# Performance work log

Hardware: AMD Instinct MI355X
Metric: run time of the kernel (lower is better)

The kernel has to match this reference:

```python
import jax, jax.numpy as jnp
import numpy as np

# model hyperparameters (from init_kwargs)
N_IN = 2048
NN = 512
BATCH = 64
DT, TAU_M, TAU_X = 0.05, 10.0, 2.0
ALPHA = 1.0 - DT / TAU_M   # membrane decay
BETA = 1.0 - DT / TAU_X    # lateral-trace decay
V_TH = 2.0


def _loo_idx(nn):
    # leave-one-out gather indices: idx[j, n] = j if j < n else j + 1
    j = np.arange(nn - 1)[:, None]
    n = np.arange(nn)[None, :]
    return jnp.asarray(j + (j >= n))  # (nn-1, nn) int


def setup_inputs() -> dict:
    key = jax.random.key(0)
    k1, k2, k3, k4 = jax.random.split(key, 4)
    x = jax.random.uniform(k1, (BATCH, N_IN, NN), dtype=jnp.float32)      # per-neuron external input
    v = jax.random.normal(k2, (BATCH, NN), dtype=jnp.float32)             # membrane state
    z = jnp.zeros((BATCH, NN), dtype=jnp.float32)                         # previous spikes
    z_out = jax.random.uniform(k3, (BATCH, NN), dtype=jnp.float32)        # lateral spike trace
    w = jax.random.normal(k4, (N_IN + NN - 1, NN), dtype=jnp.float32) / np.sqrt(N_IN)
    return {"x": x, "v": v, "z": z, "z_out": z_out, "w": w}


def reference(x, v, z, z_out, w):
    # update lateral trace: z_out = beta * z_out + z (z detached in original)
    z_out_new = BETA * z_out + z
    # leave-one-out lateral input: z_loo[b, j, n] = z_out_new[b, j + (j >= n)]
    idx = _loo_idx(NN)
    z_loo = z_out_new[:, idx]  # (B, NN-1, NN)
    # membrane drive: sum_k x_tot[b,k,n] * w[k,n], where x_tot = cat([x, z_loo], dim=1)
    drive = (jnp.einsum('bkn,kn->bn', x, w[:N_IN])
             + jnp.einsum('bjn,jn->bn', z_loo, w[N_IN:]))
    v_new = ALPHA * v + drive - V_TH * z
    # thresholding nonlinearity -> output spikes
    z_new = (v_new - V_TH > 0).astype(v.dtype)
    return v_new, z_new, z_out_new
```

## Files before the change

### kernel.cpp

```cpp
#include <hip/hip_runtime.h>

#define BATCH 64
#define N_IN  2048
#define NN    512
#define G     4
#define ALPHA 0.995f
#define BETA  0.975f
#define V_TH  2.0f

__global__ __launch_bounds__(1024, 8)
void k1_stream(const float* __restrict__ x, const float* __restrict__ w,
               const float* __restrict__ z, const float* __restrict__ z_out,
               float4* __restrict__ ws)
{
    __shared__ __align__(16) float4 red[G][8][128];
    const int kr  = blockIdx.x;
    const int b0  = blockIdx.y * G;
    const int tid = threadIdx.x;
    const int c4  = tid & 127;
    const int kl  = tid >> 7;

    const float4* __restrict__ x4 = (const float4*)x;
    const float4* __restrict__ w4 = (const float4*)w;
    const int k0 = kr * 64 + kl;

    size_t xoff[G];
#pragma unroll
    for (int g = 0; g < G; ++g)
        xoff[g] = ((size_t)(b0 + g) * N_IN + k0) * 128 + c4;
    size_t woff = (size_t)k0 * 128 + c4;
    const size_t kstep = 8 * 128;

    float4 acc[G];
#pragma unroll
    for (int g = 0; g < G; ++g) acc[g] = make_float4(0.f, 0.f, 0.f, 0.f);

#pragma unroll 2
    for (int i = 0; i < 8; ++i) {
        float4 xv[G];
#pragma unroll
        for (int g = 0; g < G; ++g) xv[g] = x4[xoff[g]];
        const float4 wv = w4[woff];
#pragma unroll
        for (int g = 0; g < G; ++g) {
            acc[g].x += xv[g].x * wv.x;
            acc[g].y += xv[g].y * wv.y;
            acc[g].z += xv[g].z * wv.z;
            acc[g].w += xv[g].w * wv.w;
        }
#pragma unroll
        for (int g = 0; g < G; ++g) xoff[g] += kstep;
        woff += kstep;
    }

#pragma unroll
    for (int g = 0; g < G; ++g) red[g][kl][c4] = acc[g];
    __syncthreads();

    float4 s = make_float4(0.f, 0.f, 0.f, 0.f);
    if (tid < 512) {
        const int g = tid >> 7, c = tid & 127;
        s = red[g][0][c];
#pragma unroll
        for (int l = 1; l < 8; ++l) {
            const float4 o = red[g][l][c];
            s.x += o.x; s.y += o.y; s.z += o.z; s.w += o.w;
        }
    }
    __syncthreads();

    float* d2l = (float*)red;
    float* zr  = d2l + G * NN;
    const int j0 = kr * 16;

    if (tid < G * 17) {
        const int g = tid / 17, jj = tid % 17;
        const int idx = j0 + jj;
        if (idx < NN)
            zr[g * 17 + jj] = BETA * z_out[(b0 + g) * NN + idx]
                            + z[(b0 + g) * NN + idx];
    }
    __syncthreads();

    {
        const int n  = tid & 511;
        const int gh = tid >> 9;
        float p0 = 0.f, p1 = 0.f;
        const int jend = (j0 + 16 < NN - 1) ? j0 + 16 : NN - 1;
        for (int j = j0; j < jend; ++j) {
            const float wv = w[(size_t)(N_IN + j) * NN + n];
            const int jj = j + (j >= n) - j0;
            p0 += zr[(gh * 2 + 0) * 17 + jj] * wv;
            p1 += zr[(gh * 2 + 1) * 17 + jj] * wv;
        }
        d2l[(gh * 2 + 0) * NN + n] = p0;
        d2l[(gh * 2 + 1) * NN + n] = p1;
    }
    __syncthreads();

    if (tid < 512) {
        const int g = tid >> 7, c = tid & 127;
        s.x += d2l[g * NN + 4 * c + 0];
        s.y += d2l[g * NN + 4 * c + 1];
        s.z += d2l[g * NN + 4 * c + 2];
        s.w += d2l[g * NN + 4 * c + 3];
        ws[((size_t)kr * BATCH + b0 + g) * 128 + c] = s;
    }
}

__global__ __launch_bounds__(128)
void k3_epi(const float* __restrict__ v, const float* __restrict__ z,
            const float* __restrict__ z_out, const float* __restrict__ ws,
            float* __restrict__ out)
{
    const int i = blockIdx.x * 128 + threadIdx.x;
    float d = 0.f;
#pragma unroll
    for (int kr = 0; kr < 32; ++kr)
        d += ws[(size_t)kr * (BATCH * NN) + i];
    const float zz = z[i];
    const float vn = ALPHA * v[i] + d - V_TH * zz;
    out[i]                  = vn;
    out[BATCH * NN + i]     = (vn - V_TH > 0.f) ? 1.f : 0.f;
    out[2 * BATCH * NN + i] = BETA * z_out[i] + zz;
}

__global__ __launch_bounds__(1024, 8)
void k1_fallback(const float* __restrict__ x, const float* __restrict__ w,
                 float4* __restrict__ ws)
{
    const int nc  = blockIdx.x;
    const int b0  = blockIdx.y * G;
    const int kr  = blockIdx.z;
    const int tid = threadIdx.x;
    const int nl  = tid & 15;
    const int kk  = tid >> 4;
    const int wid  = tid >> 6;
    const int lane = tid & 63;

    const float4* __restrict__ x4 = (const float4*)x;
    const float4* __restrict__ w4 = (const float4*)w;
    const int c4    = nc * 16 + nl;
    const int kbase = kr * 512 + kk;

    size_t xoff[G];
#pragma unroll
    for (int g = 0; g < G; ++g)
        xoff[g] = ((size_t)(b0 + g) * N_IN + kbase) * 128 + c4;
    size_t woff = (size_t)kbase * 128 + c4;
    const size_t kstep = (size_t)64 * 128;

    float4 acc[G];
#pragma unroll
    for (int g = 0; g < G; ++g) acc[g] = make_float4(0.f, 0.f, 0.f, 0.f);

#pragma unroll 2
    for (int i = 0; i < 8; ++i) {
        float4 xv[G];
#pragma unroll
        for (int g = 0; g < G; ++g) xv[g] = x4[xoff[g]];
        const float4 wv = w4[woff];
#pragma unroll
        for (int g = 0; g < G; ++g) {
            acc[g].x += xv[g].x * wv.x;
            acc[g].y += xv[g].y * wv.y;
            acc[g].z += xv[g].z * wv.z;
            acc[g].w += xv[g].w * wv.w;
        }
#pragma unroll
        for (int g = 0; g < G; ++g) xoff[g] += kstep;
        woff += kstep;
    }

#pragma unroll
    for (int off = 32; off >= 16; off >>= 1) {
#pragma unroll
        for (int g = 0; g < G; ++g) {
            acc[g].x += __shfl_down(acc[g].x, off);
            acc[g].y += __shfl_down(acc[g].y, off);
            acc[g].z += __shfl_down(acc[g].z, off);
            acc[g].w += __shfl_down(acc[g].w, off);
        }
    }

    __shared__ float4 wpart[16][G][16];
    if (lane < 16) {
#pragma unroll
        for (int g = 0; g < G; ++g) wpart[wid][g][lane] = acc[g];
    }
    __syncthreads();

    if (tid < 64) {
        const int g = tid >> 4, c = tid & 15;
        float4 sf = wpart[0][g][c];
#pragma unroll
        for (int ww = 1; ww < 16; ++ww) {
            const float4 o = wpart[ww][g][c];
            sf.x += o.x; sf.y += o.y; sf.z += o.z; sf.w += o.w;
        }
        ws[((size_t)kr * BATCH + b0 + g) * 128 + nc * 16 + c] = sf;
    }
}

__global__ __launch_bounds__(1024)
void k2_finish(const float* __restrict__ v, const float* __restrict__ z,
               const float* __restrict__ z_out, const float* __restrict__ w,
               const float* __restrict__ ws, float* __restrict__ out)
{
    const int nc  = blockIdx.x;
    const int b   = blockIdx.y;
    const int nb  = nc * 64;
    const int tid = threadIdx.x;

    __shared__ float zlds[NN];
    __shared__ float r2[1024];

    if (tid < NN)
        zlds[tid] = BETA * z_out[b * NN + tid] + z[b * NN + tid];
    __syncthreads();

    const int n_loc = tid & 63;
    const int n     = nb + n_loc;
    const int jg    = tid >> 6;
    float d2 = 0.f;
#pragma unroll 4
    for (int j = jg; j < NN - 1; j += 16)
        d2 += zlds[j + (j >= n)] * w[(size_t)(N_IN + j) * NN + n];
    r2[tid] = d2;
    __syncthreads();

    if (tid < 64) {
        float d1 = 0.f;
#pragma unroll
        for (int kr = 0; kr < 4; ++kr)
            d1 += ws[((size_t)kr * BATCH + b) * NN + n];
        float d2s = 0.f;
#pragma unroll
        for (int g = 0; g < 16; ++g) d2s += r2[g * 64 + n_loc];
        const float vv    = v[b * NN + n];
        const float zz    = z[b * NN + n];
        const float v_new = ALPHA * vv + d1 + d2s - V_TH * zz;
        out[b * NN + n]                  = v_new;
        out[BATCH * NN + b * NN + n]     = (v_new - V_TH > 0.f) ? 1.f : 0.f;
        out[2 * BATCH * NN + b * NN + n] = zlds[n];
    }
}

extern "C" void kernel_launch(void* const* d_in, const int* in_sizes, int n_in,
                              void* d_out, int out_size, void* d_ws, size_t ws_size,
                              hipStream_t stream) {
    (void)in_sizes; (void)n_in; (void)out_size;
    const float* x     = (const float*)d_in[0];
    const float* v     = (const float*)d_in[1];
    const float* z     = (const float*)d_in[2];
    const float* z_out = (const float*)d_in[3];
    const float* w     = (const float*)d_in[4];
    float* out = (float*)d_out;
    float* wsf = (float*)d_ws;

    const size_t need32 = (size_t)32 * BATCH * NN * sizeof(float);
    if (ws_size >= need32) {
        dim3 g1(32, BATCH / G);
        k1_stream<<<g1, 1024, 0, stream>>>(x, w, z, z_out, (float4*)wsf);
        k3_epi<<<BATCH * NN / 128, 128, 0, stream>>>(v, z, z_out, wsf, out);
    } else {
        dim3 g1(8, BATCH / G, 4);
        k1_fallback<<<g1, 1024, 0, stream>>>(x, w, (float4*)wsf);
        dim3 g2(8, BATCH);
        k2_finish<<<g2, 1024, 0, stream>>>(v, z, z_out, w, wsf, out);
    }
}
```

Before: 49.73 us.

## Add 8-batch-per-block stream kernel with finer K split and 64-way epilogue

Adds a new main-path kernel in which each block handles 8 batches over 32 k-rows instead of 4 batches over 64. Each loaded w vector is therefore reused across twice as many batch rows, and the lateral leave-one-out part is split into 8-column chunks. This cuts w traffic, but it doubles the partial-sum workspace (64 slices) and makes the epilogue kernel read twice as many partials. The new path is used only when the workspace is large enough; otherwise the old 4-batch kernel still runs.

```diff
diff --git a/kernel.cpp b/kernel.cpp
--- a/kernel.cpp
+++ b/kernel.cpp
@@ -3,58 +3,175 @@
 #define BATCH 64
 #define N_IN  2048
 #define NN    512
-#define G     4
 #define ALPHA 0.995f
 #define BETA  0.975f
 #define V_TH  2.0f
 
 __global__ __launch_bounds__(1024, 8)
-void k1_stream(const float* __restrict__ x, const float* __restrict__ w,
-               const float* __restrict__ z, const float* __restrict__ z_out,
-               float4* __restrict__ ws)
-{
-    __shared__ __align__(16) float4 red[G][8][128];
+void k1_stream8(const float* __restrict__ x, const float* __restrict__ w,
+                const float* __restrict__ z, const float* __restrict__ z_out,
+                float4* __restrict__ ws)
+{
+    __shared__ __align__(16) float4 red[4][8][128];
     const int kr  = blockIdx.x;
-    const int b0  = blockIdx.y * G;
+    const int b0  = blockIdx.y * 8;
     const int tid = threadIdx.x;
     const int c4  = tid & 127;
     const int kl  = tid >> 7;
+    const int k0  = kr * 32 + kl;
 
     const float4* __restrict__ x4 = (const float4*)x;
     const float4* __restrict__ w4 = (const float4*)w;
-    const int k0 = kr * 64 + kl;
-
-    size_t xoff[G];
-#pragma unroll
-    for (int g = 0; g < G; ++g)
+
+    size_t xbase = ((size_t)b0 * N_IN + k0) * 128 + c4;
+    const size_t gstr  = (size_t)N_IN * 128;
+    size_t woff  = (size_t)k0 * 128 + c4;
+    const size_t kstep = 8 * 128;
+
+    float4 acc[8];
+#pragma unroll
+    for (int g = 0; g < 8; ++g) acc[g] = make_float4(0.f, 0.f, 0.f, 0.f);
+
+#pragma unroll
+    for (int i = 0; i < 4; ++i) {
+        float4 xv[4];
+#pragma unroll
+        for (int u = 0; u < 4; ++u) xv[u] = x4[xbase + u * gstr];
+        const float4 wv = w4[woff];
+#pragma unroll
+        for (int u = 0; u < 4; ++u) {
+            acc[u].x += xv[u].x * wv.x;  acc[u].y += xv[u].y * wv.y;
+            acc[u].z += xv[u].z * wv.z;  acc[u].w += xv[u].w * wv.w;
+        }
+#pragma unroll
+        for (int u = 0; u < 4; ++u) xv[u] = x4[xbase + (4 + u) * gstr];
+#pragma unroll
+        for (int u = 0; u < 4; ++u) {
+            acc[4+u].x += xv[u].x * wv.x;  acc[4+u].y += xv[u].y * wv.y;
+            acc[4+u].z += xv[u].z * wv.z;  acc[4+u].w += xv[u].w * wv.w;
+        }
+        xbase += kstep;
+        woff  += kstep;
+    }
+
+    float4 s0 = make_float4(0.f, 0.f, 0.f, 0.f);
+    float4 s1 = make_float4(0.f, 0.f, 0.f, 0.f);
+    const int gg = tid >> 7, cc = tid & 127;
+
+#pragma unroll
+    for (int q = 0; q < 4; ++q) red[q][kl][c4] = acc[q];
+    __syncthreads();
+    if (tid < 512) {
+        s0 = red[gg][0][cc];
+#pragma unroll
+        for (int l = 1; l < 8; ++l) {
+            const float4 o = red[gg][l][cc];
+            s0.x += o.x; s0.y += o.y; s0.z += o.z; s0.w += o.w;
+        }
+    }
+    __syncthreads();
+#pragma unroll
+    for (int q = 0; q < 4; ++q) red[q][kl][c4] = acc[4 + q];
+    __syncthreads();
+    if (tid < 512) {
+        s1 = red[gg][0][cc];
+#pragma unroll
+        for (int l = 1; l < 8; ++l) {
+            const float4 o = red[gg][l][cc];
+            s1.x += o.x; s1.y += o.y; s1.z += o.z; s1.w += o.w;
+        }
+    }
+    __syncthreads();
+
+    float* d2l = (float*)red;
+    float* zr  = d2l + 8 * NN;
+    const int j0 = kr * 8;
+
+    if (tid < 8 * 9) {
+        const int g = tid / 9, jj = tid % 9;
+        const int idx = j0 + jj;
+        if (idx < NN)
+            zr[g * 9 + jj] = BETA * z_out[(b0 + g) * NN + idx]
+                           + z[(b0 + g) * NN + idx];
+    }
+    __syncthreads();
+
+    {
+        const int n  = tid & 511;
+        const int gh = tid >> 9;
+        float p[4] = {0.f, 0.f, 0.f, 0.f};
+        const int jend = (j0 + 8 < NN - 1) ? j0 + 8 : NN - 1;
+        for (int j = j0; j < jend; ++j) {
+            const float wv = w[(size_t)(N_IN + j) * NN + n];
+            const int jj = j + (j >= n) - j0;
+#pragma unroll
+            for (int q = 0; q < 4; ++q)
+                p[q] += zr[(gh * 4 + q) * 9 + jj] * wv;
+        }
+#pragma unroll
+        for (int q = 0; q < 4; ++q) d2l[(gh * 4 + q) * NN + n] = p[q];
+    }
+    __syncthreads();
+
+    if (tid < 512) {
+        s0.x += d2l[gg * NN + 4 * cc + 0];
+        s0.y += d2l[gg * NN + 4 * cc + 1];
+        s0.z += d2l[gg * NN + 4 * cc + 2];
+        s0.w += d2l[gg * NN + 4 * cc + 3];
+        s1.x += d2l[(4 + gg) * NN + 4 * cc + 0];
+        s1.y += d2l[(4 + gg) * NN + 4 * cc + 1];
+        s1.z += d2l[(4 + gg) * NN + 4 * cc + 2];
+        s1.w += d2l[(4 + gg) * NN + 4 * cc + 3];
+        ws[((size_t)kr * BATCH + b0 + gg) * 128 + cc]     = s0;
+        ws[((size_t)kr * BATCH + b0 + 4 + gg) * 128 + cc] = s1;
+    }
+}
+
+__global__ __launch_bounds__(1024, 8)
+void k1_stream4(const float* __restrict__ x, const float* __restrict__ w,
+                const float* __restrict__ z, const float* __restrict__ z_out,
+                float4* __restrict__ ws)
+{
+    __shared__ __align__(16) float4 red[4][8][128];
+    const int kr  = blockIdx.x;
+    const int b0  = blockIdx.y * 4;
+    const int tid = threadIdx.x;
+    const int c4  = tid & 127;
+    const int kl  = tid >> 7;
+    const int k0  = kr * 64 + kl;
+
+    const float4* __restrict__ x4 = (const float4*)x;
+    const float4* __restrict__ w4 = (const float4*)w;
+
+    size_t xoff[4];
+#pragma unroll
+    for (int g = 0; g < 4; ++g)
         xoff[g] = ((size_t)(b0 + g) * N_IN + k0) * 128 + c4;
     size_t woff = (size_t)k0 * 128 + c4;
     const size_t kstep = 8 * 128;
 
-    float4 acc[G];
-#pragma unroll
-    for (int g = 0; g < G; ++g) acc[g] = make_float4(0.f, 0.f, 0.f, 0.f);
+    float4 acc[4];
+#pragma unroll
+    for (int g = 0; g < 4; ++g) acc[g] = make_float4(0.f, 0.f, 0.f, 0.f);
 
 #pragma unroll 2
     for (int i = 0; i < 8; ++i) {
-        float4 xv[G];
-#pragma unroll
-        for (int g = 0; g < G; ++g) xv[g] = x4[xoff[g]];
+        float4 xv[4];
+#pragma unroll
+        for (int g = 0; g < 4; ++g) xv[g] = x4[xoff[g]];
         const float4 wv = w4[woff];
 #pragma unroll
-        for (int g = 0; g < G; ++g) {
-            acc[g].x += xv[g].x * wv.x;
-            acc[g].y += xv[g].y * wv.y;
-            acc[g].z += xv[g].z * wv.z;
-            acc[g].w += xv[g].w * wv.w;
-        }
-#pragma unroll
-        for (int g = 0; g < G; ++g) xoff[g] += kstep;
+        for (int g = 0; g < 4; ++g) {
+            acc[g].x += xv[g].x * wv.x;  acc[g].y += xv[g].y * wv.y;
+            acc[g].z += xv[g].z * wv.z;  acc[g].w += xv[g].w * wv.w;
+        }
+#pragma unroll
+        for (int g = 0; g < 4; ++g) xoff[g] += kstep;
         woff += kstep;
     }
 
 #pragma unroll
-    for (int g = 0; g < G; ++g) red[g][kl][c4] = acc[g];
+    for (int g = 0; g < 4; ++g) red[g][kl][c4] = acc[g];
     __syncthreads();
 
     float4 s = make_float4(0.f, 0.f, 0.f, 0.f);
@@ -70,10 +187,10 @@
     __syncthreads();
 
     float* d2l = (float*)red;
-    float* zr  = d2l + G * NN;
+    float* zr  = d2l + 4 * NN;
     const int j0 = kr * 16;
 
-    if (tid < G * 17) {
+    if (tid < 4 * 17) {
         const int g = tid / 17, jj = tid % 17;
         const int idx = j0 + jj;
         if (idx < NN)
@@ -108,6 +225,7 @@
     }
 }
 
+template <int KRV>
 __global__ __launch_bounds__(128)
 void k3_epi(const float* __restrict__ v, const float* __restrict__ z,
             const float* __restrict__ z_out, const float* __restrict__ ws,
@@ -116,7 +234,7 @@
     const int i = blockIdx.x * 128 + threadIdx.x;
     float d = 0.f;
 #pragma unroll
-    for (int kr = 0; kr < 32; ++kr)
+    for (int kr = 0; kr < KRV; ++kr)
         d += ws[(size_t)kr * (BATCH * NN) + i];
     const float zz = z[i];
     const float vn = ALPHA * v[i] + d - V_TH * zz;
@@ -130,7 +248,7 @@
                  float4* __restrict__ ws)
 {
     const int nc  = blockIdx.x;
-    const int b0  = blockIdx.y * G;
+    const int b0  = blockIdx.y * 4;
     const int kr  = blockIdx.z;
     const int tid = threadIdx.x;
     const int nl  = tid & 15;
@@ -143,39 +261,37 @@
     const int c4    = nc * 16 + nl;
     const int kbase = kr * 512 + kk;
 
-    size_t xoff[G];
-#pragma unroll
-    for (int g = 0; g < G; ++g)
+    size_t xoff[4];
+#pragma unroll
+    for (int g = 0; g < 4; ++g)
         xoff[g] = ((size_t)(b0 + g) * N_IN + kbase) * 128 + c4;
     size_t woff = (size_t)kbase * 128 + c4;
     const size_t kstep = (size_t)64 * 128;
 
-    float4 acc[G];
-#pragma unroll
-    for (int g = 0; g < G; ++g) acc[g] = make_float4(0.f, 0.f, 0.f, 0.f);
+    float4 acc[4];
+#pragma unroll
+    for (int g = 0; g < 4; ++g) acc[g] = make_float4(0.f, 0.f, 0.f, 0.f);
 
 #pragma unroll 2
     for (int i = 0; i < 8; ++i) {
-        float4 xv[G];
-#pragma unroll
-        for (int g = 0; g < G; ++g) xv[g] = x4[xoff[g]];
+        float4 xv[4];
+#pragma unroll
+        for (int g = 0; g < 4; ++g) xv[g] = x4[xoff[g]];
         const float4 wv = w4[woff];
 #pragma unroll
-        for (int g = 0; g < G; ++g) {
-            acc[g].x += xv[g].x * wv.x;
-            acc[g].y += xv[g].y * wv.y;
-            acc[g].z += xv[g].z * wv.z;
-            acc[g].w += xv[g].w * wv.w;
-        }
-#pragma unroll
-        for (int g = 0; g < G; ++g) xoff[g] += kstep;
+        for (int g = 0; g < 4; ++g) {
+            acc[g].x += xv[g].x * wv.x;  acc[g].y += xv[g].y * wv.y;
+            acc[g].z += xv[g].z * wv.z;  acc[g].w += xv[g].w * wv.w;
+        }
+#pragma unroll
+        for (int g = 0; g < 4; ++g) xoff[g] += kstep;
         woff += kstep;
     }
 
 #pragma unroll
     for (int off = 32; off >= 16; off >>= 1) {
 #pragma unroll
-        for (int g = 0; g < G; ++g) {
+        for (int g = 0; g < 4; ++g) {
             acc[g].x += __shfl_down(acc[g].x, off);
             acc[g].y += __shfl_down(acc[g].y, off);
             acc[g].z += __shfl_down(acc[g].z, off);
@@ -183,10 +299,10 @@
         }
     }
 
-    __shared__ float4 wpart[16][G][16];
+    __shared__ float4 wpart[16][4][16];
     if (lane < 16) {
 #pragma unroll
-        for (int g = 0; g < G; ++g) wpart[wid][g][lane] = acc[g];
+        for (int g = 0; g < 4; ++g) wpart[wid][g][lane] = acc[g];
     }
     __syncthreads();
 
@@ -258,13 +374,18 @@
     float* out = (float*)d_out;
     float* wsf = (float*)d_ws;
 
+    const size_t need64 = (size_t)64 * BATCH * NN * sizeof(float);
     const size_t need32 = (size_t)32 * BATCH * NN * sizeof(float);
-    if (ws_size >= need32) {
-        dim3 g1(32, BATCH / G);
-        k1_stream<<<g1, 1024, 0, stream>>>(x, w, z, z_out, (float4*)wsf);
-        k3_epi<<<BATCH * NN / 128, 128, 0, stream>>>(v, z, z_out, wsf, out);
+    if (ws_size >= need64) {
+        dim3 g1(64, 8);
+        k1_stream8<<<g1, 1024, 0, stream>>>(x, w, z, z_out, (float4*)wsf);
+        k3_epi<64><<<BATCH * NN / 128, 128, 0, stream>>>(v, z, z_out, wsf, out);
+    } else if (ws_size >= need32) {
+        dim3 g1(32, 16);
+        k1_stream4<<<g1, 1024, 0, stream>>>(x, w, z, z_out, (float4*)wsf);
+        k3_epi<32><<<BATCH * NN / 128, 128, 0, stream>>>(v, z, z_out, wsf, out);
     } else {
-        dim3 g1(8, BATCH / G, 4);
+        dim3 g1(8, 16, 4);
         k1_fallback<<<g1, 1024, 0, stream>>>(x, w, (float4*)wsf);
         dim3 g2(8, BATCH);
         k2_finish<<<g2, 1024, 0, stream>>>(v, z, z_out, w, wsf, out);
```

Result: slower. 115.1 us (+131.5%).
